# Optimization experiments

Measured on AMD Instinct MI355X. Metric: run time of the kernel, lower is better.

The kernel has to match this reference:

```python
import jax, jax.numpy as jnp
import numpy as np

N_NODES = 100000
N_EDGES = 1600000
HIDDEN = 128
LAYERS = 2


def setup_inputs() -> dict:
    key = jax.random.key(0)
    k1, k2, k3, k4 = jax.random.split(key, 4)
    x = jax.random.normal(k1, (N_NODES, HIDDEN), dtype=jnp.float32)
    edge_index = jax.random.randint(k2, (2, N_EDGES), 0, N_NODES, dtype=jnp.int32)
    # Glorot-ish init for per-layer GCN weights, small bias
    Ws = jax.random.normal(k3, (LAYERS, HIDDEN, HIDDEN), dtype=jnp.float32) / np.sqrt(HIDDEN).astype(np.float32)
    bs = jax.random.normal(k4, (LAYERS, HIDDEN), dtype=jnp.float32) * 0.01
    return {"x": x, "edge_index": edge_index, "Ws": Ws, "bs": bs}


def reference(x, edge_index, Ws, bs):
    # PyG GCNConv with normalize=True, add_self_loops=False:
    #   x' = D^{-1/2} A D^{-1/2} (x W) + b,  deg = in-degree at target (col) nodes
    src = edge_index[0]  # message sources (row)
    dst = edge_index[1]  # message targets (col), aggregation index
    ones = jnp.ones(src.shape[0], dtype=x.dtype)
    deg = jax.ops.segment_sum(ones, dst, num_segments=N_NODES)
    dinv = jnp.where(deg > 0, jax.lax.rsqrt(jnp.maximum(deg, 1.0)), jnp.zeros_like(deg))
    norm = dinv[src] * dinv[dst]  # [E] symmetric edge normalization
    for l in range(Ws.shape[0]):
        h = x @ Ws[l]                                  # [N, D] dense transform
        msg = h[src] * norm[:, None]                   # [E, D] gather + scale
        x = jax.ops.segment_sum(msg, dst, num_segments=N_NODES) + bs[l]
    return x
```

## Files before the change

### kernel.cpp

```cpp
#include <hip/hip_runtime.h>

#define HID 128
#define WFRAG (HID*HID)

typedef __attribute__((ext_vector_type(8))) short bf16x8;
typedef __attribute__((ext_vector_type(4))) float f32x4;

static __device__ __forceinline__ unsigned short f2bf(float f){
  unsigned u = __float_as_uint(f);
  unsigned r = (u + 0x7FFF + ((u >> 16) & 1)) >> 16;
  return (unsigned short)r;
}
static __device__ __forceinline__ float bf2f_lo(unsigned u){ return __uint_as_float(u << 16); }
static __device__ __forceinline__ float bf2f_hi(unsigned u){ return __uint_as_float(u & 0xFFFF0000u); }

static __device__ __forceinline__ unsigned cvtpk(float lo, float hi){
  unsigned r;
  asm volatile("v_cvt_pk_bf16_f32 %0, %1, %2" : "=v"(r) : "v"(lo), "v"(hi));
  return r;
}

static __device__ __forceinline__ void wprep_body(int layer, const float* __restrict__ Ws,
                                                  unsigned short* __restrict__ Whi,
                                                  unsigned short* __restrict__ Wlo){
  const float* W = Ws + (size_t)layer*HID*HID;
  for (int idx = threadIdx.x; idx < 2048; idx += 256){
    int lane = idx & 63, kstep = (idx>>6)&3, nblk = idx>>8;
    int col = 16*nblk + (lane&15);
    int k0  = 32*kstep + 8*(lane>>4);
    size_t obase = ((size_t)(layer*8 + nblk)*4 + kstep)*512 + (size_t)lane*8;
    for (int j = 0; j < 8; j++){
      float v = W[(size_t)(k0+j)*HID + col];
      unsigned short h = f2bf(v);
      float hf = __uint_as_float((unsigned)h << 16);
      Whi[obase+j] = h;
      Wlo[obase+j] = f2bf(v - hf);
    }
  }
}

__global__ __launch_bounds__(256) void k_pos_wprep(const int* __restrict__ dst, int* __restrict__ fill,
                                                   int* __restrict__ pos, int E, int L,
                                                   const float* __restrict__ Ws,
                                                   unsigned short* __restrict__ Whi,
                                                   unsigned short* __restrict__ Wlo){
  int bid = blockIdx.x;
  if (bid < L){ wprep_body(bid, Ws, Whi, Wlo); return; }
  int e = (bid - L)*256 + threadIdx.x;
  if (e < E) pos[e] = atomicAdd(&fill[dst[e]], 1);
}

__global__ __launch_bounds__(256) void k_alloc(const int* __restrict__ deg, int* __restrict__ rowstart,
                                               float* __restrict__ dinv, int* __restrict__ cursor, int N){
  __shared__ int sm[256];
  __shared__ int sbase;
  int t = threadIdx.x;
  int n = blockIdx.x*256 + t;
  int d = (n < N) ? deg[n] : 0;
  sm[t] = d;
  __syncthreads();
  for (int off = 1; off < 256; off <<= 1){
    int v = (t >= off) ? sm[t-off] : 0;
    __syncthreads();
    sm[t] += v;
    __syncthreads();
  }
  if (t == 255) sbase = atomicAdd(cursor, sm[255]);
  __syncthreads();
  if (n < N){
    rowstart[n] = sbase + sm[t] - d;
    dinv[n] = d > 0 ? rsqrtf((float)d) : 0.0f;
  }
}

static __device__ __forceinline__ void gemm_body(int bid, const float* __restrict__ X,
                                                 const unsigned short* __restrict__ Whi,
                                                 const unsigned short* __restrict__ Wlo,
                                                 const float* __restrict__ dinv,
                                                 unsigned short* __restrict__ H2u, int N){
  int t = threadIdx.x, w = t>>6, l = t&63;
  int row0 = bid*32;
  int lrow = l & 15, lk = (l>>4)*8;
  f32x4 acc[2][2] = {};
#pragma unroll 1
  for (int kstep = 0; kstep < 4; kstep++){
    bf16x8 ahi[2], alo[2];
#pragma unroll
    for (int m = 0; m < 2; m++){
      int row = row0 + 16*m + lrow;
      if (row >= N) row = N-1;
      const float* ap = X + (size_t)row*HID + kstep*32 + lk;
      float4 a0 = *(const float4*)ap;
      float4 a1 = *(const float4*)(ap+4);
      int4 hh, ll;
      hh.x = cvtpk(a0.x, a0.y); hh.y = cvtpk(a0.z, a0.w);
      hh.z = cvtpk(a1.x, a1.y); hh.w = cvtpk(a1.z, a1.w);
      ll.x = cvtpk(a0.x - bf2f_lo(hh.x), a0.y - bf2f_hi(hh.x));
      ll.y = cvtpk(a0.z - bf2f_lo(hh.y), a0.w - bf2f_hi(hh.y));
      ll.z = cvtpk(a1.x - bf2f_lo(hh.z), a1.y - bf2f_hi(hh.z));
      ll.w = cvtpk(a1.z - bf2f_lo(hh.w), a1.w - bf2f_hi(hh.w));
      ahi[m] = *(bf16x8*)&hh;
      alo[m] = *(bf16x8*)&ll;
    }
    bf16x8 bhi[2], blo[2];
#pragma unroll
    for (int n = 0; n < 2; n++){
      size_t base = ((size_t)((2*w+n)*4 + kstep))*512 + (size_t)l*8;
      bhi[n] = *(const bf16x8*)(Whi + base);
      blo[n] = *(const bf16x8*)(Wlo + base);
    }
#pragma unroll
    for (int m = 0; m < 2; m++)
#pragma unroll
      for (int n = 0; n < 2; n++){
        acc[m][n] = __builtin_amdgcn_mfma_f32_16x16x32_bf16(ahi[m], bhi[n], acc[m][n], 0, 0, 0);
        acc[m][n] = __builtin_amdgcn_mfma_f32_16x16x32_bf16(alo[m], bhi[n], acc[m][n], 0, 0, 0);
        acc[m][n] = __builtin_amdgcn_mfma_f32_16x16x32_bf16(ahi[m], blo[n], acc[m][n], 0, 0, 0);
      }
  }
#pragma unroll
  for (int m = 0; m < 2; m++)
#pragma unroll
    for (int r = 0; r < 4; r++){
      int row = row0 + 16*m + 4*(l>>4) + r;
      if (row < N){
        float dv = dinv[row];
#pragma unroll
        for (int n = 0; n < 2; n++){
          int col = 16*(2*w+n) + lrow;
          H2u[(size_t)row*HID + col] = f2bf(dv * acc[m][n][r]);
        }
      }
    }
}

__global__ __launch_bounds__(256) void k_gemm_scatter(const float* __restrict__ X,
                                                      const unsigned short* __restrict__ Whi,
                                                      const unsigned short* __restrict__ Wlo,
                                                      const float* __restrict__ dinv,
                                                      unsigned short* __restrict__ H2u, int N, int Gg,
                                                      const int* __restrict__ src, const int* __restrict__ dst,
                                                      const int* __restrict__ pos, const int* __restrict__ rowstart,
                                                      int* __restrict__ slots, int E){
  int bid = blockIdx.x;
  if (bid < Gg){ gemm_body(bid, X, Whi, Wlo, dinv, H2u, N); return; }
  int i0 = ((bid - Gg)*256 + threadIdx.x)*2;
  if (i0 + 1 < E){
    int2 s = *(const int2*)(src + i0);
    int2 d = *(const int2*)(dst + i0);
    int2 p = *(const int2*)(pos + i0);
    slots[rowstart[d.x] + p.x] = s.x;
    slots[rowstart[d.y] + p.y] = s.y;
  } else if (i0 < E){
    slots[rowstart[dst[i0]] + pos[i0]] = src[i0];
  }
}

__global__ __launch_bounds__(256) void k_gemm_mfma(const float* __restrict__ X,
                                                   const unsigned short* __restrict__ Whi,
                                                   const unsigned short* __restrict__ Wlo,
                                                   const float* __restrict__ dinv,
                                                   unsigned short* __restrict__ H2u, int N){
  gemm_body(blockIdx.x, X, Whi, Wlo, dinv, H2u, N);
}

__global__ __launch_bounds__(256) void k_agg(const uint4* __restrict__ H4, const int* __restrict__ slots,
                                             const int* __restrict__ rowstart, const int* __restrict__ deg,
                                             const float* __restrict__ dinv,
                                             const float* __restrict__ bias, float* __restrict__ out, int N){
  int wid = threadIdx.x >> 6, lane = threadIdx.x & 63;
  int n = blockIdx.x*4 + wid;
  if (n >= N) return;
  int st = rowstart[n], cnt = deg[n];
  int g = lane >> 4, c = lane & 15;
  float a[8] = {0.f,0.f,0.f,0.f,0.f,0.f,0.f,0.f};
  for (int j = 0; j < cnt; j += 16){
    int cl = cnt - 1;
    int ix[4];
#pragma unroll
    for (int q = 0; q < 4; q++){
      int jj = j + 4*q + g;
      ix[q] = slots[st + (jj < cnt ? jj : cl)];
    }
    uint4 v[4];
#pragma unroll
    for (int q = 0; q < 4; q++) v[q] = H4[(size_t)ix[q]*16 + c];
#pragma unroll
    for (int q = 0; q < 4; q++){
      if (j + 4*q + g >= cnt){ v[q].x=0u; v[q].y=0u; v[q].z=0u; v[q].w=0u; }
      a[0] += bf2f_lo(v[q].x);
      a[1] += bf2f_hi(v[q].x);
      a[2] += bf2f_lo(v[q].y);
      a[3] += bf2f_hi(v[q].y);
      a[4] += bf2f_lo(v[q].z);
      a[5] += bf2f_hi(v[q].z);
      a[6] += bf2f_lo(v[q].w);
      a[7] += bf2f_hi(v[q].w);
    }
  }
#pragma unroll
  for (int q = 0; q < 8; q++){
    a[q] += __shfl_xor(a[q], 16);
    a[q] += __shfl_xor(a[q], 32);
  }
  if (g == 0){
    float dv = dinv[n];
    const float4* b4 = (const float4*)bias;
    float4 b0 = b4[c*2], b1 = b4[c*2+1];
    float4 o0 = make_float4(dv*a[0]+b0.x, dv*a[1]+b0.y, dv*a[2]+b0.z, dv*a[3]+b0.w);
    float4 o1 = make_float4(dv*a[4]+b1.x, dv*a[5]+b1.y, dv*a[6]+b1.z, dv*a[7]+b1.w);
    float4* orow = (float4*)(out + (size_t)n*HID);
    orow[c*2]   = o0;
    orow[c*2+1] = o1;
  }
}

extern "C" void kernel_launch(void* const* d_in, const int* in_sizes, int n_in,
                              void* d_out, int out_size, void* d_ws, size_t ws_size,
                              hipStream_t stream){
  const float* x  = (const float*)d_in[0];
  const int*   ei = (const int*)d_in[1];
  const float* Ws = (const float*)d_in[2];
  const float* bs = (const float*)d_in[3];
  const int N = in_sizes[0] / HID;
  const int E = in_sizes[1] / 2;
  const int L = in_sizes[2] / (HID*HID);
  const int* src = ei;
  const int* dst = ei + E;
  const int NB = (N + 255)/256;

  char* w = (char*)d_ws;
  int*   fill     = (int*)w;   w += (size_t)N*4;
  int*   cursor   = (int*)w;   w += 16;
  size_t zbytes = (size_t)(w - (char*)d_ws);
  float* dinv     = (float*)w; w += (size_t)N*4;
  int*   rowstart = (int*)w;   w += (size_t)N*4;
  int*   pos      = (int*)w;   w += (size_t)E*4;
  int*   slots    = (int*)w;   w += (size_t)E*4 + 64;
  unsigned short* h2u = (unsigned short*)w; w += (size_t)N*HID*2;
  unsigned short* whi = (unsigned short*)w; w += (size_t)L*WFRAG*2;
  unsigned short* wlo = (unsigned short*)w; w += (size_t)L*WFRAG*2;

  hipMemsetAsync(d_ws, 0, zbytes, stream);

  int gE  = (E + 255)/256;
  int Gs  = (E/2 + 255)/256 + 1;
  int Gg  = (N + 31)/32;
  k_pos_wprep<<<gE + L, 256, 0, stream>>>(dst, fill, pos, E, L, Ws, whi, wlo);
  k_alloc    <<<NB, 256, 0, stream>>>(fill, rowstart, dinv, cursor, N);
  k_gemm_scatter<<<Gg + Gs, 256, 0, stream>>>(x, whi, wlo, dinv, h2u, N, Gg,
                                              src, dst, pos, rowstart, slots, E);
  float* out = (float*)d_out;
  k_agg<<<(N + 3)/4, 256, 0, stream>>>((const uint4*)h2u, slots, rowstart, fill,
                                       dinv, bs, out, N);
  for (int l = 1; l < L; l++){
    k_gemm_mfma<<<Gg, 256, 0, stream>>>(out, whi + (size_t)l*WFRAG, wlo + (size_t)l*WFRAG,
                                        dinv, h2u, N);
    k_agg<<<(N + 3)/4, 256, 0, stream>>>((const uint4*)h2u, slots, rowstart, fill,
                                         dinv, bs + (size_t)l*HID, out, N);
  }
}
```

Before: 332.9 us.

## Overlap layer-0 GEMM with degree counting; store bf16 intermediate; per-edge weights in slots

```diff
diff --git a/kernel.cpp b/kernel.cpp
--- a/kernel.cpp
+++ b/kernel.cpp
@@ -20,9 +20,10 @@
   return r;
 }
 
-static __device__ __forceinline__ void wprep_body(int layer, const float* __restrict__ Ws,
-                                                  unsigned short* __restrict__ Whi,
-                                                  unsigned short* __restrict__ Wlo){
+__global__ __launch_bounds__(256) void k_wprep(const float* __restrict__ Ws,
+                                               unsigned short* __restrict__ Whi,
+                                               unsigned short* __restrict__ Wlo){
+  int layer = blockIdx.x;
   const float* W = Ws + (size_t)layer*HID*HID;
   for (int idx = threadIdx.x; idx < 2048; idx += 256){
     int lane = idx & 63, kstep = (idx>>6)&3, nblk = idx>>8;
@@ -39,45 +40,10 @@
   }
 }
 
-__global__ __launch_bounds__(256) void k_pos_wprep(const int* __restrict__ dst, int* __restrict__ fill,
-                                                   int* __restrict__ pos, int E, int L,
-                                                   const float* __restrict__ Ws,
-                                                   unsigned short* __restrict__ Whi,
-                                                   unsigned short* __restrict__ Wlo){
-  int bid = blockIdx.x;
-  if (bid < L){ wprep_body(bid, Ws, Whi, Wlo); return; }
-  int e = (bid - L)*256 + threadIdx.x;
-  if (e < E) pos[e] = atomicAdd(&fill[dst[e]], 1);
-}
-
-__global__ __launch_bounds__(256) void k_alloc(const int* __restrict__ deg, int* __restrict__ rowstart,
-                                               float* __restrict__ dinv, int* __restrict__ cursor, int N){
-  __shared__ int sm[256];
-  __shared__ int sbase;
-  int t = threadIdx.x;
-  int n = blockIdx.x*256 + t;
-  int d = (n < N) ? deg[n] : 0;
-  sm[t] = d;
-  __syncthreads();
-  for (int off = 1; off < 256; off <<= 1){
-    int v = (t >= off) ? sm[t-off] : 0;
-    __syncthreads();
-    sm[t] += v;
-    __syncthreads();
-  }
-  if (t == 255) sbase = atomicAdd(cursor, sm[255]);
-  __syncthreads();
-  if (n < N){
-    rowstart[n] = sbase + sm[t] - d;
-    dinv[n] = d > 0 ? rsqrtf((float)d) : 0.0f;
-  }
-}
-
-static __device__ __forceinline__ void gemm_body(int bid, const float* __restrict__ X,
-                                                 const unsigned short* __restrict__ Whi,
-                                                 const unsigned short* __restrict__ Wlo,
-                                                 const float* __restrict__ dinv,
-                                                 unsigned short* __restrict__ H2u, int N){
+static __device__ __forceinline__ void gemm_body_f32(int bid, const float* __restrict__ X,
+                                                     const unsigned short* __restrict__ Whi,
+                                                     const unsigned short* __restrict__ Wlo,
+                                                     unsigned short* __restrict__ H2u, int N){
   int t = threadIdx.x, w = t>>6, l = t&63;
   int row0 = bid*32;
   int lrow = l & 15, lk = (l>>4)*8;
@@ -102,21 +68,18 @@
       ahi[m] = *(bf16x8*)&hh;
       alo[m] = *(bf16x8*)&ll;
     }
-    bf16x8 bhi[2], blo[2];
 #pragma unroll
     for (int n = 0; n < 2; n++){
       size_t base = ((size_t)((2*w+n)*4 + kstep))*512 + (size_t)l*8;
-      bhi[n] = *(const bf16x8*)(Whi + base);
-      blo[n] = *(const bf16x8*)(Wlo + base);
-    }
-#pragma unroll
-    for (int m = 0; m < 2; m++)
-#pragma unroll
-      for (int n = 0; n < 2; n++){
-        acc[m][n] = __builtin_amdgcn_mfma_f32_16x16x32_bf16(ahi[m], bhi[n], acc[m][n], 0, 0, 0);
-        acc[m][n] = __builtin_amdgcn_mfma_f32_16x16x32_bf16(alo[m], bhi[n], acc[m][n], 0, 0, 0);
-        acc[m][n] = __builtin_amdgcn_mfma_f32_16x16x32_bf16(ahi[m], blo[n], acc[m][n], 0, 0, 0);
+      bf16x8 bhi = *(const bf16x8*)(Whi + base);
+      bf16x8 blo = *(const bf16x8*)(Wlo + base);
+#pragma unroll
+      for (int m = 0; m < 2; m++){
+        acc[m][n] = __builtin_amdgcn_mfma_f32_16x16x32_bf16(ahi[m], bhi, acc[m][n], 0, 0, 0);
+        acc[m][n] = __builtin_amdgcn_mfma_f32_16x16x32_bf16(alo[m], bhi, acc[m][n], 0, 0, 0);
+        acc[m][n] = __builtin_amdgcn_mfma_f32_16x16x32_bf16(ahi[m], blo, acc[m][n], 0, 0, 0);
       }
+    }
   }
 #pragma unroll
   for (int m = 0; m < 2; m++)
@@ -124,50 +87,119 @@
     for (int r = 0; r < 4; r++){
       int row = row0 + 16*m + 4*(l>>4) + r;
       if (row < N){
-        float dv = dinv[row];
 #pragma unroll
         for (int n = 0; n < 2; n++){
           int col = 16*(2*w+n) + lrow;
-          H2u[(size_t)row*HID + col] = f2bf(dv * acc[m][n][r]);
+          H2u[(size_t)row*HID + col] = f2bf(acc[m][n][r]);
         }
       }
     }
 }
 
-__global__ __launch_bounds__(256) void k_gemm_scatter(const float* __restrict__ X,
-                                                      const unsigned short* __restrict__ Whi,
-                                                      const unsigned short* __restrict__ Wlo,
-                                                      const float* __restrict__ dinv,
-                                                      unsigned short* __restrict__ H2u, int N, int Gg,
-                                                      const int* __restrict__ src, const int* __restrict__ dst,
-                                                      const int* __restrict__ pos, const int* __restrict__ rowstart,
-                                                      int* __restrict__ slots, int E){
+__global__ __launch_bounds__(256) void k_pos_gemm0(const int* __restrict__ dst, int* __restrict__ fill,
+                                                   int* __restrict__ pos, int E, int Gp,
+                                                   const unsigned short* __restrict__ Whi,
+                                                   const unsigned short* __restrict__ Wlo,
+                                                   const float* __restrict__ X,
+                                                   unsigned short* __restrict__ H2u, int N){
   int bid = blockIdx.x;
-  if (bid < Gg){ gemm_body(bid, X, Whi, Wlo, dinv, H2u, N); return; }
-  int i0 = ((bid - Gg)*256 + threadIdx.x)*2;
+  if (bid < Gp){
+    int e = bid*256 + threadIdx.x;
+    if (e < E) pos[e] = atomicAdd(&fill[dst[e]], 1);
+    return;
+  }
+  gemm_body_f32(bid - Gp, X, Whi, Wlo, H2u, N);
+}
+
+__global__ __launch_bounds__(256) void k_alloc(const int* __restrict__ deg, int* __restrict__ rowstart,
+                                               float* __restrict__ dinv, int* __restrict__ cursor, int N){
+  __shared__ int sm[256];
+  __shared__ int sbase;
+  int t = threadIdx.x;
+  int n = blockIdx.x*256 + t;
+  int d = (n < N) ? deg[n] : 0;
+  sm[t] = d;
+  __syncthreads();
+  for (int off = 1; off < 256; off <<= 1){
+    int v = (t >= off) ? sm[t-off] : 0;
+    __syncthreads();
+    sm[t] += v;
+    __syncthreads();
+  }
+  if (t == 255) sbase = atomicAdd(cursor, sm[255]);
+  __syncthreads();
+  if (n < N){
+    rowstart[n] = sbase + sm[t] - d;
+    dinv[n] = d > 0 ? rsqrtf((float)d) : 0.0f;
+  }
+}
+
+__global__ __launch_bounds__(256) void k_scatter(const int* __restrict__ src, const int* __restrict__ dst,
+                                                 const int* __restrict__ pos, const int* __restrict__ rowstart,
+                                                 const float* __restrict__ dinv,
+                                                 int2* __restrict__ slots, int E){
+  int i0 = (blockIdx.x*256 + threadIdx.x)*2;
   if (i0 + 1 < E){
     int2 s = *(const int2*)(src + i0);
     int2 d = *(const int2*)(dst + i0);
     int2 p = *(const int2*)(pos + i0);
-    slots[rowstart[d.x] + p.x] = s.x;
-    slots[rowstart[d.y] + p.y] = s.y;
+    slots[rowstart[d.x] + p.x] = make_int2(s.x, __float_as_int(dinv[s.x]));
+    slots[rowstart[d.y] + p.y] = make_int2(s.y, __float_as_int(dinv[s.y]));
   } else if (i0 < E){
-    slots[rowstart[dst[i0]] + pos[i0]] = src[i0];
-  }
-}
-
-__global__ __launch_bounds__(256) void k_gemm_mfma(const float* __restrict__ X,
+    int s = src[i0];
+    slots[rowstart[dst[i0]] + pos[i0]] = make_int2(s, __float_as_int(dinv[s]));
+  }
+}
+
+__global__ __launch_bounds__(256) void k_gemm_bf16(const unsigned short* __restrict__ Xb,
                                                    const unsigned short* __restrict__ Whi,
                                                    const unsigned short* __restrict__ Wlo,
-                                                   const float* __restrict__ dinv,
                                                    unsigned short* __restrict__ H2u, int N){
-  gemm_body(blockIdx.x, X, Whi, Wlo, dinv, H2u, N);
-}
-
-__global__ __launch_bounds__(256) void k_agg(const uint4* __restrict__ H4, const int* __restrict__ slots,
+  int t = threadIdx.x, w = t>>6, l = t&63;
+  int row0 = blockIdx.x*32;
+  int lrow = l & 15, lk = (l>>4)*8;
+  f32x4 acc[2][2] = {};
+#pragma unroll 1
+  for (int kstep = 0; kstep < 4; kstep++){
+    bf16x8 a[2];
+#pragma unroll
+    for (int m = 0; m < 2; m++){
+      int row = row0 + 16*m + lrow;
+      if (row >= N) row = N-1;
+      a[m] = *(const bf16x8*)(Xb + (size_t)row*HID + kstep*32 + lk);
+    }
+#pragma unroll
+    for (int n = 0; n < 2; n++){
+      size_t base = ((size_t)((2*w+n)*4 + kstep))*512 + (size_t)l*8;
+      bf16x8 bhi = *(const bf16x8*)(Whi + base);
+      bf16x8 blo = *(const bf16x8*)(Wlo + base);
+#pragma unroll
+      for (int m = 0; m < 2; m++){
+        acc[m][n] = __builtin_amdgcn_mfma_f32_16x16x32_bf16(a[m], bhi, acc[m][n], 0, 0, 0);
+        acc[m][n] = __builtin_amdgcn_mfma_f32_16x16x32_bf16(a[m], blo, acc[m][n], 0, 0, 0);
+      }
+    }
+  }
+#pragma unroll
+  for (int m = 0; m < 2; m++)
+#pragma unroll
+    for (int r = 0; r < 4; r++){
+      int row = row0 + 16*m + 4*(l>>4) + r;
+      if (row < N){
+#pragma unroll
+        for (int n = 0; n < 2; n++){
+          int col = 16*(2*w+n) + lrow;
+          H2u[(size_t)row*HID + col] = f2bf(acc[m][n][r]);
+        }
+      }
+    }
+}
+
+template<int OUTBF>
+__global__ __launch_bounds__(256) void k_agg(const uint4* __restrict__ H4, const int2* __restrict__ slots,
                                              const int* __restrict__ rowstart, const int* __restrict__ deg,
                                              const float* __restrict__ dinv,
-                                             const float* __restrict__ bias, float* __restrict__ out, int N){
+                                             const float* __restrict__ bias, void* __restrict__ outp, int N){
   int wid = threadIdx.x >> 6, lane = threadIdx.x & 63;
   int n = blockIdx.x*4 + wid;
   if (n >= N) return;
@@ -176,26 +208,26 @@
   float a[8] = {0.f,0.f,0.f,0.f,0.f,0.f,0.f,0.f};
   for (int j = 0; j < cnt; j += 16){
     int cl = cnt - 1;
-    int ix[4];
+    int2 sl[4];
 #pragma unroll
     for (int q = 0; q < 4; q++){
       int jj = j + 4*q + g;
-      ix[q] = slots[st + (jj < cnt ? jj : cl)];
+      sl[q] = slots[st + (jj < cnt ? jj : cl)];
     }
     uint4 v[4];
 #pragma unroll
-    for (int q = 0; q < 4; q++) v[q] = H4[(size_t)ix[q]*16 + c];
+    for (int q = 0; q < 4; q++) v[q] = H4[(size_t)sl[q].x*16 + c];
 #pragma unroll
     for (int q = 0; q < 4; q++){
-      if (j + 4*q + g >= cnt){ v[q].x=0u; v[q].y=0u; v[q].z=0u; v[q].w=0u; }
-      a[0] += bf2f_lo(v[q].x);
-      a[1] += bf2f_hi(v[q].x);
-      a[2] += bf2f_lo(v[q].y);
-      a[3] += bf2f_hi(v[q].y);
-      a[4] += bf2f_lo(v[q].z);
-      a[5] += bf2f_hi(v[q].z);
-      a[6] += bf2f_lo(v[q].w);
-      a[7] += bf2f_hi(v[q].w);
+      float wq = (j + 4*q + g < cnt) ? __int_as_float(sl[q].y) : 0.f;
+      a[0] += wq*bf2f_lo(v[q].x);
+      a[1] += wq*bf2f_hi(v[q].x);
+      a[2] += wq*bf2f_lo(v[q].y);
+      a[3] += wq*bf2f_hi(v[q].y);
+      a[4] += wq*bf2f_lo(v[q].z);
+      a[5] += wq*bf2f_hi(v[q].z);
+      a[6] += wq*bf2f_lo(v[q].w);
+      a[7] += wq*bf2f_hi(v[q].w);
     }
   }
 #pragma unroll
@@ -207,11 +239,21 @@
     float dv = dinv[n];
     const float4* b4 = (const float4*)bias;
     float4 b0 = b4[c*2], b1 = b4[c*2+1];
-    float4 o0 = make_float4(dv*a[0]+b0.x, dv*a[1]+b0.y, dv*a[2]+b0.z, dv*a[3]+b0.w);
-    float4 o1 = make_float4(dv*a[4]+b1.x, dv*a[5]+b1.y, dv*a[6]+b1.z, dv*a[7]+b1.w);
-    float4* orow = (float4*)(out + (size_t)n*HID);
-    orow[c*2]   = o0;
-    orow[c*2+1] = o1;
+    float o[8];
+    o[0]=dv*a[0]+b0.x; o[1]=dv*a[1]+b0.y; o[2]=dv*a[2]+b0.z; o[3]=dv*a[3]+b0.w;
+    o[4]=dv*a[4]+b1.x; o[5]=dv*a[5]+b1.y; o[6]=dv*a[6]+b1.z; o[7]=dv*a[7]+b1.w;
+    if (OUTBF){
+      uint4 p;
+      p.x = (unsigned)f2bf(o[0]) | ((unsigned)f2bf(o[1]) << 16);
+      p.y = (unsigned)f2bf(o[2]) | ((unsigned)f2bf(o[3]) << 16);
+      p.z = (unsigned)f2bf(o[4]) | ((unsigned)f2bf(o[5]) << 16);
+      p.w = (unsigned)f2bf(o[6]) | ((unsigned)f2bf(o[7]) << 16);
+      ((uint4*)outp)[(size_t)n*16 + c] = p;
+    } else {
+      float4* orow = (float4*)((float*)outp + (size_t)n*HID);
+      orow[c*2]   = make_float4(o[0],o[1],o[2],o[3]);
+      orow[c*2+1] = make_float4(o[4],o[5],o[6],o[7]);
+    }
   }
 }
 
@@ -236,27 +278,28 @@
   float* dinv     = (float*)w; w += (size_t)N*4;
   int*   rowstart = (int*)w;   w += (size_t)N*4;
   int*   pos      = (int*)w;   w += (size_t)E*4;
-  int*   slots    = (int*)w;   w += (size_t)E*4 + 64;
+  int2*  slots    = (int2*)w;  w += (size_t)E*8 + 64;
   unsigned short* h2u = (unsigned short*)w; w += (size_t)N*HID*2;
+  unsigned short* xb1 = (unsigned short*)w; w += (size_t)N*HID*2;
   unsigned short* whi = (unsigned short*)w; w += (size_t)L*WFRAG*2;
   unsigned short* wlo = (unsigned short*)w; w += (size_t)L*WFRAG*2;
 
   hipMemsetAsync(d_ws, 0, zbytes, stream);
 
-  int gE  = (E + 255)/256;
-  int Gs  = (E/2 + 255)/256 + 1;
-  int Gg  = (N + 31)/32;
-  k_pos_wprep<<<gE + L, 256, 0, stream>>>(dst, fill, pos, E, L, Ws, whi, wlo);
+  int Gp = (E + 255)/256;
+  int Gs = (E/2 + 255)/256 + 1;
+  int Gg = (N + 31)/32;
+  int Ga = (N + 3)/4;
+
+  k_wprep    <<<L, 256, 0, stream>>>(Ws, whi, wlo);
+  k_pos_gemm0<<<Gp + Gg, 256, 0, stream>>>(dst, fill, pos, E, Gp,
+                                           whi, wlo, x, h2u, N);
   k_alloc    <<<NB, 256, 0, stream>>>(fill, rowstart, dinv, cursor, N);
-  k_gemm_scatter<<<Gg + Gs, 256, 0, stream>>>(x, whi, wlo, dinv, h2u, N, Gg,
-                                              src, dst, pos, rowstart, slots, E);
-  float* out = (float*)d_out;
-  k_agg<<<(N + 3)/4, 256, 0, stream>>>((const uint4*)h2u, slots, rowstart, fill,
-                                       dinv, bs, out, N);
-  for (int l = 1; l < L; l++){
-    k_gemm_mfma<<<Gg, 256, 0, stream>>>(out, whi + (size_t)l*WFRAG, wlo + (size_t)l*WFRAG,
-                                        dinv, h2u, N);
-    k_agg<<<(N + 3)/4, 256, 0, stream>>>((const uint4*)h2u, slots, rowstart, fill,
-                                         dinv, bs + (size_t)l*HID, out, N);
-  }
-}
+  k_scatter  <<<Gs, 256, 0, stream>>>(src, dst, pos, rowstart, dinv, slots, E);
+
+  k_agg<1><<<Ga, 256, 0, stream>>>((const uint4*)h2u, slots, rowstart, fill,
+                                   dinv, bs, (void*)xb1, N);
+  k_gemm_bf16<<<Gg, 256, 0, stream>>>(xb1, whi + WFRAG, wlo + WFRAG, h2u, N);
+  k_agg<0><<<Ga, 256, 0, stream>>>((const uint4*)h2u, slots, rowstart, fill,
+                                   dinv, bs + HID, d_out, N);
+}
```

After: 331.3 us. Within noise of the previous version (-0.5%).
